# Performance work log

Hardware: AMD Instinct MI355X
Metric: run time of the kernel (lower is better)

## Reference

```python
import jax, jax.numpy as jnp
import numpy as np

ND_WEIGHT = 1.0
NUM_CLASS = 1000
B, D = 16384, 2048


def setup_inputs() -> dict:
    key = jax.random.key(0)
    k1, k2, k3, k4 = jax.random.split(key, 4)
    s_emb = jax.random.normal(k1, (B, D), dtype=jnp.float32)
    t_emb = jax.random.normal(k2, (B, D), dtype=jnp.float32)
    T_EMB = jax.random.normal(k3, (NUM_CLASS, D), dtype=jnp.float32)
    labels = jax.random.randint(k4, (B,), 0, NUM_CLASS, dtype=jnp.int64)
    return {"s_emb": s_emb, "t_emb": t_emb, "T_EMB": T_EMB, "labels": labels}


def reference(s_emb, t_emb, T_EMB, labels):
    # Gather per-sample class centers: [B, D]
    centers = T_EMB[labels]
    # Unit-normalize each center (L2 along feature dim)
    e_c = centers / jnp.linalg.norm(centers, axis=-1, keepdims=True)
    # Per-sample max of student/teacher embedding norms: [B]
    s_norm = jnp.linalg.norm(s_emb, axis=-1)
    t_norm = jnp.linalg.norm(t_emb, axis=-1)
    max_norm = jnp.maximum(s_norm, t_norm)
    # 1 - <s, e_c> / max_norm, summed then averaged, scaled by nd_weight
    dots = jnp.sum(s_emb * e_c, axis=-1)
    loss_sum = jnp.sum(1.0 - dots / max_norm)
    return loss_sum * ND_WEIGHT / s_emb.shape[0]
```

## Files before the change

kernel.cpp:

```cpp
#include <hip/hip_runtime.h>


#define NROWS  16384
#define DDIM   2048
#define BLK    256
#define WPB    (BLK / 64)
#define GRID   (NROWS / WPB)

__global__ __launch_bounds__(BLK, 2) void dnl_main_kernel(
    const float* __restrict__ s_emb,
    const float* __restrict__ t_emb,
    const float* __restrict__ T_EMB,
    const int*   __restrict__ labels,
    float*       __restrict__ partial)
{
    const int tid  = threadIdx.x;
    const int lane = tid & 63;
    const int row  = blockIdx.x * WPB + (tid >> 6);

    const int label = labels[row];

    const float4* s4 = (const float4*)(s_emb + (size_t)row   * DDIM);
    const float4* t4 = (const float4*)(t_emb + (size_t)row   * DDIM);
    const float4* c4 = (const float4*)(T_EMB + (size_t)label * DDIM);

    float4 sv[8], tv[8], cv[8];
    #pragma unroll
    for (int j = 0; j < 8; ++j) sv[j] = s4[lane + j * 64];
    #pragma unroll
    for (int j = 0; j < 8; ++j) tv[j] = t4[lane + j * 64];
    #pragma unroll
    for (int j = 0; j < 8; ++j) cv[j] = c4[lane + j * 64];

    float ss = 0.f, tt = 0.f, sc = 0.f, cc = 0.f;
    #pragma unroll
    for (int j = 0; j < 8; ++j) {
        const float4 s = sv[j], t = tv[j], c = cv[j];
        ss += s.x*s.x + s.y*s.y + s.z*s.z + s.w*s.w;
        tt += t.x*t.x + t.y*t.y + t.z*t.z + t.w*t.w;
        sc += s.x*c.x + s.y*c.y + s.z*c.z + s.w*c.w;
        cc += c.x*c.x + c.y*c.y + c.z*c.z + c.w*c.w;
    }

    #pragma unroll
    for (int off = 32; off > 0; off >>= 1) {
        ss += __shfl_xor(ss, off, 64);
        tt += __shfl_xor(tt, off, 64);
        sc += __shfl_xor(sc, off, 64);
        cc += __shfl_xor(cc, off, 64);
    }

    if (lane == 0) {
        const float max_norm = fmaxf(sqrtf(ss), sqrtf(tt));
        partial[row] = 1.0f - sc / (sqrtf(cc) * max_norm);
    }
}

__global__ __launch_bounds__(BLK) void dnl_reduce_kernel(
    const float* __restrict__ partial,
    float*       __restrict__ out)
{
    const int tid = threadIdx.x;
    const float4* p4 = (const float4*)partial;
    float sum = 0.f;
    #pragma unroll
    for (int j = 0; j < 16; ++j) {
        const float4 v = p4[tid + j * BLK];
        sum += v.x + v.y + v.z + v.w;
    }

    #pragma unroll
    for (int off = 32; off > 0; off >>= 1)
        sum += __shfl_xor(sum, off, 64);

    __shared__ float red[4];
    if ((tid & 63) == 0) red[tid >> 6] = sum;
    __syncthreads();
    if (tid == 0)
        out[0] = (red[0] + red[1] + red[2] + red[3]) * (1.0f / (float)NROWS);
}

__global__ __launch_bounds__(BLK, 2) void dnl_main_atomic_kernel(
    const float* __restrict__ s_emb,
    const float* __restrict__ t_emb,
    const float* __restrict__ T_EMB,
    const int*   __restrict__ labels,
    float*       __restrict__ out)
{
    const int tid  = threadIdx.x;
    const int lane = tid & 63;
    const int row  = blockIdx.x * WPB + (tid >> 6);
    const int label = labels[row];

    const float4* s4 = (const float4*)(s_emb + (size_t)row   * DDIM);
    const float4* t4 = (const float4*)(t_emb + (size_t)row   * DDIM);
    const float4* c4 = (const float4*)(T_EMB + (size_t)label * DDIM);

    float4 sv[8], tv[8], cv[8];
    #pragma unroll
    for (int j = 0; j < 8; ++j) sv[j] = s4[lane + j * 64];
    #pragma unroll
    for (int j = 0; j < 8; ++j) tv[j] = t4[lane + j * 64];
    #pragma unroll
    for (int j = 0; j < 8; ++j) cv[j] = c4[lane + j * 64];

    float ss = 0.f, tt = 0.f, sc = 0.f, cc = 0.f;
    #pragma unroll
    for (int j = 0; j < 8; ++j) {
        const float4 s = sv[j], t = tv[j], c = cv[j];
        ss += s.x*s.x + s.y*s.y + s.z*s.z + s.w*s.w;
        tt += t.x*t.x + t.y*t.y + t.z*t.z + t.w*t.w;
        sc += s.x*c.x + s.y*c.y + s.z*c.z + s.w*c.w;
        cc += c.x*c.x + c.y*c.y + c.z*c.z + c.w*c.w;
    }
    #pragma unroll
    for (int off = 32; off > 0; off >>= 1) {
        ss += __shfl_xor(ss, off, 64);
        tt += __shfl_xor(tt, off, 64);
        sc += __shfl_xor(sc, off, 64);
        cc += __shfl_xor(cc, off, 64);
    }
    if (lane == 0) {
        const float max_norm = fmaxf(sqrtf(ss), sqrtf(tt));
        atomicAdd(out, (1.0f - sc / (sqrtf(cc) * max_norm)) * (1.0f / (float)NROWS));
    }
}

extern "C" void kernel_launch(void* const* d_in, const int* in_sizes, int n_in,
                              void* d_out, int out_size, void* d_ws, size_t ws_size,
                              hipStream_t stream) {
    const float* s_emb  = (const float*)d_in[0];
    const float* t_emb  = (const float*)d_in[1];
    const float* T_EMB  = (const float*)d_in[2];
    const int*   labels = (const int*)d_in[3];
    float* out = (float*)d_out;

    if (ws_size >= (size_t)NROWS * sizeof(float)) {
        float* partial = (float*)d_ws;
        dnl_main_kernel<<<GRID, BLK, 0, stream>>>(s_emb, t_emb, T_EMB, labels, partial);
        dnl_reduce_kernel<<<1, BLK, 0, stream>>>(partial, out);
    } else {
        hipMemsetAsync(d_out, 0, sizeof(float), stream);
        dnl_main_atomic_kernel<<<GRID, BLK, 0, stream>>>(s_emb, t_emb, T_EMB, labels, out);
    }
}
```

Before: 287.7 us.

## Sort rows by label so each wave reuses the class center across rows

```diff
diff --git a/kernel.cpp b/kernel.cpp
--- a/kernel.cpp
+++ b/kernel.cpp
@@ -3,76 +3,134 @@
 
 #define NROWS  16384
 #define DDIM   2048
+#define NCLS   1000
+#define NBIN   1024
 #define BLK    256
-#define WPB    (BLK / 64)
-#define GRID   (NROWS / WPB)
-
-__global__ __launch_bounds__(BLK, 2) void dnl_main_kernel(
+#define CHUNK  4
+#define NWAVES (NROWS / CHUNK)
+#define MGRID  (NWAVES / (BLK / 64))
+
+#define WS_CNT    0
+#define WS_CUR    (NBIN)
+#define WS_SORTED (2 * NBIN)
+#define WS_WSUM   (2 * NBIN + NROWS)
+#define WS_NEEDED ((size_t)(2 * NBIN + NROWS + NWAVES) * 4)
+
+__global__ void dnl_zero_kernel(int* __restrict__ cnt) {
+    const int i = blockIdx.x * blockDim.x + threadIdx.x;
+    if (i < NBIN) cnt[i] = 0;
+}
+
+__global__ void dnl_histo_kernel(const int* __restrict__ labels,
+                                 int* __restrict__ cnt) {
+    const int i = blockIdx.x * blockDim.x + threadIdx.x;
+    if (i < NROWS) atomicAdd(&cnt[labels[i]], 1);
+}
+
+__global__ __launch_bounds__(NBIN) void dnl_scan_kernel(
+    const int* __restrict__ cnt, int* __restrict__ cur) {
+    __shared__ int a[NBIN], b[NBIN];
+    const int tid = threadIdx.x;
+    a[tid] = cnt[tid];
+    __syncthreads();
+    int* src = a; int* dst = b;
+    for (int d = 1; d < NBIN; d <<= 1) {
+        dst[tid] = (tid >= d) ? src[tid] + src[tid - d] : src[tid];
+        __syncthreads();
+        int* tmp = src; src = dst; dst = tmp;
+    }
+    cur[tid] = src[tid] - cnt[tid];
+}
+
+__global__ void dnl_scatter_kernel(const int* __restrict__ labels,
+                                   int* __restrict__ cur,
+                                   int* __restrict__ sorted) {
+    const int i = blockIdx.x * blockDim.x + threadIdx.x;
+    if (i < NROWS) {
+        const int p = atomicAdd(&cur[labels[i]], 1);
+        sorted[p] = i;
+    }
+}
+
+__global__ __launch_bounds__(BLK) void dnl_main_sorted(
     const float* __restrict__ s_emb,
     const float* __restrict__ t_emb,
     const float* __restrict__ T_EMB,
     const int*   __restrict__ labels,
-    float*       __restrict__ partial)
+    const int*   __restrict__ sorted,
+    float*       __restrict__ wavesum)
 {
     const int tid  = threadIdx.x;
     const int lane = tid & 63;
-    const int row  = blockIdx.x * WPB + (tid >> 6);
-
-    const int label = labels[row];
-
-    const float4* s4 = (const float4*)(s_emb + (size_t)row   * DDIM);
-    const float4* t4 = (const float4*)(t_emb + (size_t)row   * DDIM);
-    const float4* c4 = (const float4*)(T_EMB + (size_t)label * DDIM);
-
-    float4 sv[8], tv[8], cv[8];
-    #pragma unroll
-    for (int j = 0; j < 8; ++j) sv[j] = s4[lane + j * 64];
-    #pragma unroll
-    for (int j = 0; j < 8; ++j) tv[j] = t4[lane + j * 64];
-    #pragma unroll
-    for (int j = 0; j < 8; ++j) cv[j] = c4[lane + j * 64];
-
-    float ss = 0.f, tt = 0.f, sc = 0.f, cc = 0.f;
-    #pragma unroll
-    for (int j = 0; j < 8; ++j) {
-        const float4 s = sv[j], t = tv[j], c = cv[j];
-        ss += s.x*s.x + s.y*s.y + s.z*s.z + s.w*s.w;
-        tt += t.x*t.x + t.y*t.y + t.z*t.z + t.w*t.w;
-        sc += s.x*c.x + s.y*c.y + s.z*c.z + s.w*c.w;
-        cc += c.x*c.x + c.y*c.y + c.z*c.z + c.w*c.w;
-    }
-
-    #pragma unroll
-    for (int off = 32; off > 0; off >>= 1) {
-        ss += __shfl_xor(ss, off, 64);
-        tt += __shfl_xor(tt, off, 64);
-        sc += __shfl_xor(sc, off, 64);
-        cc += __shfl_xor(cc, off, 64);
-    }
-
-    if (lane == 0) {
+    const int w    = blockIdx.x * (BLK / 64) + (tid >> 6);
+
+    float4 cv[8];
+    float  ccs = 0.f;
+    int    cur_class = -1;
+    float  acc = 0.f;
+
+    for (int r = 0; r < CHUNK; ++r) {
+        const int row   = sorted[w * CHUNK + r];
+        const int label = labels[row];
+
+        if (label != cur_class) {
+            cur_class = label;
+            const float4* c4 = (const float4*)(T_EMB + (size_t)label * DDIM);
+            float cc = 0.f;
+            #pragma unroll
+            for (int j = 0; j < 8; ++j) cv[j] = c4[lane + j * 64];
+            #pragma unroll
+            for (int j = 0; j < 8; ++j) {
+                const float4 c = cv[j];
+                cc += c.x*c.x + c.y*c.y + c.z*c.z + c.w*c.w;
+            }
+            #pragma unroll
+            for (int off = 32; off > 0; off >>= 1)
+                cc += __shfl_xor(cc, off, 64);
+            ccs = cc;
+        }
+
+        const float4* s4 = (const float4*)(s_emb + (size_t)row * DDIM);
+        const float4* t4 = (const float4*)(t_emb + (size_t)row * DDIM);
+        float ss = 0.f, tt = 0.f, sc = 0.f;
+        #pragma unroll
+        for (int j = 0; j < 8; ++j) {
+            const float4 s = s4[lane + j * 64];
+            const float4 t = t4[lane + j * 64];
+            const float4 c = cv[j];
+            ss += s.x*s.x + s.y*s.y + s.z*s.z + s.w*s.w;
+            tt += t.x*t.x + t.y*t.y + t.z*t.z + t.w*t.w;
+            sc += s.x*c.x + s.y*c.y + s.z*c.z + s.w*c.w;
+        }
+        #pragma unroll
+        for (int off = 32; off > 0; off >>= 1) {
+            ss += __shfl_xor(ss, off, 64);
+            tt += __shfl_xor(tt, off, 64);
+            sc += __shfl_xor(sc, off, 64);
+        }
+
         const float max_norm = fmaxf(sqrtf(ss), sqrtf(tt));
-        partial[row] = 1.0f - sc / (sqrtf(cc) * max_norm);
-    }
+        acc += 1.0f - sc / (sqrtf(ccs) * max_norm);
+    }
+
+    if (lane == 0) wavesum[w] = acc;
 }
 
 __global__ __launch_bounds__(BLK) void dnl_reduce_kernel(
-    const float* __restrict__ partial,
+    const float* __restrict__ wavesum,
     float*       __restrict__ out)
 {
     const int tid = threadIdx.x;
-    const float4* p4 = (const float4*)partial;
+    const float4* w4 = (const float4*)wavesum;
     float sum = 0.f;
     #pragma unroll
-    for (int j = 0; j < 16; ++j) {
-        const float4 v = p4[tid + j * BLK];
+    for (int j = 0; j < NWAVES / 4 / BLK; ++j) {
+        const float4 v = w4[tid + j * BLK];
         sum += v.x + v.y + v.z + v.w;
     }
-
     #pragma unroll
     for (int off = 32; off > 0; off >>= 1)
         sum += __shfl_xor(sum, off, 64);
-
     __shared__ float red[4];
     if ((tid & 63) == 0) red[tid >> 6] = sum;
     __syncthreads();
@@ -80,7 +138,7 @@
         out[0] = (red[0] + red[1] + red[2] + red[3]) * (1.0f / (float)NROWS);
 }
 
-__global__ __launch_bounds__(BLK, 2) void dnl_main_atomic_kernel(
+__global__ __launch_bounds__(BLK) void dnl_main_atomic_kernel(
     const float* __restrict__ s_emb,
     const float* __restrict__ t_emb,
     const float* __restrict__ T_EMB,
@@ -89,25 +147,20 @@
 {
     const int tid  = threadIdx.x;
     const int lane = tid & 63;
-    const int row  = blockIdx.x * WPB + (tid >> 6);
+    const int row  = blockIdx.x * (BLK / 64) + (tid >> 6);
     const int label = labels[row];
 
     const float4* s4 = (const float4*)(s_emb + (size_t)row   * DDIM);
     const float4* t4 = (const float4*)(t_emb + (size_t)row   * DDIM);
     const float4* c4 = (const float4*)(T_EMB + (size_t)label * DDIM);
 
-    float4 sv[8], tv[8], cv[8];
-    #pragma unroll
-    for (int j = 0; j < 8; ++j) sv[j] = s4[lane + j * 64];
-    #pragma unroll
-    for (int j = 0; j < 8; ++j) tv[j] = t4[lane + j * 64];
-    #pragma unroll
-    for (int j = 0; j < 8; ++j) cv[j] = c4[lane + j * 64];
-
     float ss = 0.f, tt = 0.f, sc = 0.f, cc = 0.f;
     #pragma unroll
     for (int j = 0; j < 8; ++j) {
-        const float4 s = sv[j], t = tv[j], c = cv[j];
+        const int k = lane + j * 64;
+        const float4 s = s4[k];
+        const float4 t = t4[k];
+        const float4 c = c4[k];
         ss += s.x*s.x + s.y*s.y + s.z*s.z + s.w*s.w;
         tt += t.x*t.x + t.y*t.y + t.z*t.z + t.w*t.w;
         sc += s.x*c.x + s.y*c.y + s.z*c.z + s.w*c.w;
@@ -135,12 +188,22 @@
     const int*   labels = (const int*)d_in[3];
     float* out = (float*)d_out;
 
-    if (ws_size >= (size_t)NROWS * sizeof(float)) {
-        float* partial = (float*)d_ws;
-        dnl_main_kernel<<<GRID, BLK, 0, stream>>>(s_emb, t_emb, T_EMB, labels, partial);
-        dnl_reduce_kernel<<<1, BLK, 0, stream>>>(partial, out);
+    if (ws_size >= WS_NEEDED) {
+        int*   cnt     = (int*)d_ws + WS_CNT;
+        int*   cur     = (int*)d_ws + WS_CUR;
+        int*   sorted  = (int*)d_ws + WS_SORTED;
+        float* wavesum = (float*)d_ws + WS_WSUM;
+
+        dnl_zero_kernel   <<<(NBIN + 255) / 256, 256, 0, stream>>>(cnt);
+        dnl_histo_kernel  <<<NROWS / 256, 256, 0, stream>>>(labels, cnt);
+        dnl_scan_kernel   <<<1, NBIN, 0, stream>>>(cnt, cur);
+        dnl_scatter_kernel<<<NROWS / 256, 256, 0, stream>>>(labels, cur, sorted);
+        dnl_main_sorted   <<<MGRID, BLK, 0, stream>>>(s_emb, t_emb, T_EMB,
+                                                      labels, sorted, wavesum);
+        dnl_reduce_kernel <<<1, BLK, 0, stream>>>(wavesum, out);
     } else {
         hipMemsetAsync(d_out, 0, sizeof(float), stream);
-        dnl_main_atomic_kernel<<<GRID, BLK, 0, stream>>>(s_emb, t_emb, T_EMB, labels, out);
-    }
-}
+        dnl_main_atomic_kernel<<<NROWS / (BLK / 64), BLK, 0, stream>>>(
+            s_emb, t_emb, T_EMB, labels, out);
+    }
+}
```

Measured after the change: 308.4 us. +7.2%, slower.
